# Optimization experiments

Measured on AMD Instinct MI355X. Metric: run time of the kernel, lower is better.

## Reference

```python
import jax, jax.numpy as jnp
import numpy as np

N, E = 50000, 1600000
IN_C, HEADS, OUT_C = 128, 4, 32


def setup_inputs() -> dict:
    key = jax.random.key(0)
    ks = jax.random.split(key, 8)
    x = jax.random.normal(ks[0], (N, IN_C), dtype=jnp.float32)
    row = jnp.sort(jax.random.randint(ks[1], (E,), 0, N, dtype=jnp.int32)).astype(jnp.int64)
    col = jax.random.randint(ks[2], (E,), 0, N, dtype=jnp.int64)
    # xavier_uniform-style params
    def xavier(k, shape, fan_in, fan_out):
        lim = float(np.sqrt(6.0 / (fan_in + fan_out)))
        return jax.random.uniform(k, shape, jnp.float32, -lim, lim)
    weight = xavier(ks[3], (IN_C, HEADS * OUT_C), IN_C, HEADS * OUT_C)
    att_src = xavier(ks[4], (1, HEADS, OUT_C), HEADS, OUT_C)
    att_dst = xavier(ks[5], (1, HEADS, OUT_C), HEADS, OUT_C)
    bias = jnp.zeros((HEADS * OUT_C,), jnp.float32)
    return {"x": x, "weight": weight, "att_src": att_src, "att_dst": att_dst,
            "bias": bias, "row": row, "col": col}


def reference(x, weight, att_src, att_dst, bias, row, col):
    n = x.shape[0]
    H, C = att_src.shape[1], att_src.shape[2]
    xp = (x @ weight).reshape(n, H, C)                 # [N,H,C]
    a_src = jnp.sum(xp * att_src, axis=-1)             # [N,H]
    a_dst = jnp.sum(xp * att_dst, axis=-1)             # [N,H]
    alpha = jax.nn.leaky_relu(a_src[row] + a_dst[col], negative_slope=0.2)  # [E,H]
    # torch scatter_reduce amax with include_self=True over a zeros buffer -> max(0, seg_max)
    amax = jnp.maximum(jax.ops.segment_max(alpha, row, num_segments=n), 0.0)
    alpha = jnp.exp(alpha - amax[row])
    asum = jax.ops.segment_sum(alpha, row, num_segments=n)
    alpha = alpha / (asum[row] + 1e-8)                 # [E,H]
    msg = alpha[:, :, None] * xp[col]                  # [E,H,C]
    out = jax.ops.segment_sum(msg, row, num_segments=n).reshape(n, H * C)
    return out + bias
```

## Files before the change

### kernel.cpp

```cpp
#include <hip/hip_runtime.h>
#include <hip/hip_bf16.h>


#define IN_C 128
#define HC 128
#define STG 256

typedef __attribute__((ext_vector_type(8))) __bf16 bfrag_t;
typedef __attribute__((ext_vector_type(4))) float f32x4;
union frag_u { uint4 u; bfrag_t b; };

static __device__ inline unsigned short f2bf(float f) {
    unsigned u = __float_as_uint(f);
    unsigned r = (u + 0x7fffu + ((u >> 16) & 1u)) >> 16;
    return (unsigned short)r;
}
static __device__ inline unsigned pack2(float a, float b) {
    return (unsigned)f2bf(a) | ((unsigned)f2bf(b) << 16);
}
static __device__ inline float bf_lo(unsigned u) { return __uint_as_float(u << 16); }
static __device__ inline float bf_hi(unsigned u) { return __uint_as_float(u & 0xffff0000u); }
static __device__ inline float bfu(unsigned short s) {
    return __uint_as_float((unsigned)s << 16);
}

__global__ __launch_bounds__(256) void prep_kernel(const float* __restrict__ W,
                                                   unsigned short* __restrict__ wt,
                                                   const int* __restrict__ row,
                                                   int* __restrict__ row_ptr,
                                                   int n_nodes, int E) {
    int gid = blockIdx.x * 256 + threadIdx.x;
    if (gid < IN_C * HC) {
        int n = gid >> 7, k = gid & 127;
        wt[((size_t)n * 16 + ((k >> 3) ^ (n & 7))) * 8 + (k & 7)] =
            f2bf(W[(size_t)k * HC + n]);
    }
    if (gid < E) {
        int lane = threadIdx.x & 63;
        int r1 = row[gid];
        int r0 = __shfl_up(r1, 1, 64);
        if (lane == 0) r0 = (gid == 0) ? -1 : row[gid - 1];
        for (int v = r0 + 1; v <= r1; ++v) row_ptr[v] = gid;
        if (gid == E - 1)
            for (int v = r1 + 1; v <= n_nodes; ++v) row_ptr[v] = E;
    }
}

__global__ __launch_bounds__(512) void gemm_kernel(const float* __restrict__ x,
                                                   const uint4* __restrict__ wt,
                                                   const float* __restrict__ attS,
                                                   const float* __restrict__ attD,
                                                   unsigned short* __restrict__ xp,
                                                   float* __restrict__ a_src,
                                                   float* __restrict__ a_dst, int n_nodes) {
    __shared__ uint4 Bl[2048];
    __shared__ uint4 Al[2048];
    const int tid = threadIdx.x;
    const int base = blockIdx.x * 128;

    #pragma unroll
    for (int i = 0; i < 4; ++i) Bl[tid + 512 * i] = wt[tid + 512 * i];

    #pragma unroll
    for (int i = 0; i < 4; ++i) {
        int idx = tid + 512 * i;
        int row = idx >> 4, chunk = idx & 15;
        uint4 p = make_uint4(0u, 0u, 0u, 0u);
        if (base + row < n_nodes) {
            const float* src = x + (size_t)(base + row) * IN_C + chunk * 8;
            float4 lo = *(const float4*)src;
            float4 hi = *(const float4*)(src + 4);
            p.x = pack2(lo.x, lo.y); p.y = pack2(lo.z, lo.w);
            p.z = pack2(hi.x, hi.y); p.w = pack2(hi.z, hi.w);
        }
        Al[row * 16 + (chunk ^ (row & 7))] = p;
    }
    __syncthreads();

    const int w = tid >> 6, l = tid & 63, l15 = l & 15, q = l >> 4;
    f32x4 acc[8] = {};
    const int arow = 16 * w + l15;
    #pragma unroll
    for (int ks = 0; ks < 4; ++ks) {
        frag_u a; a.u = Al[arow * 16 + ((ks * 4 + q) ^ (arow & 7))];
        #pragma unroll
        for (int t = 0; t < 8; ++t) {
            int brow = 16 * t + l15;
            frag_u b; b.u = Bl[brow * 16 + ((ks * 4 + q) ^ (brow & 7))];
            acc[t] = __builtin_amdgcn_mfma_f32_16x16x32_bf16(a.b, b.b, acc[t], 0, 0, 0);
        }
    }

    float avS[8], avD[8];
    #pragma unroll
    for (int t = 0; t < 8; ++t) {
        avS[t] = attS[16 * t + l15];
        avD[t] = attD[16 * t + l15];
    }
    float hpS[4][4] = {}, hpD[4][4] = {};
    #pragma unroll
    for (int t = 0; t < 8; ++t) {
        #pragma unroll
        for (int r = 0; r < 4; ++r) {
            float v = acc[t][r];
            hpS[r][t >> 1] = fmaf(v, avS[t], hpS[r][t >> 1]);
            hpD[r][t >> 1] = fmaf(v, avD[t], hpD[r][t >> 1]);
            int grow = base + 16 * w + 4 * q + r;
            if (grow < n_nodes)
                xp[(size_t)grow * HC + 16 * t + l15] = f2bf(v);
        }
    }
    #pragma unroll
    for (int r = 0; r < 4; ++r) {
        #pragma unroll
        for (int h = 0; h < 4; ++h) {
            #pragma unroll
            for (int off = 1; off < 16; off <<= 1) {
                hpS[r][h] += __shfl_xor(hpS[r][h], off, 64);
                hpD[r][h] += __shfl_xor(hpD[r][h], off, 64);
            }
        }
        int grow = base + 16 * w + 4 * q + r;
        if (l15 == 0 && grow < n_nodes) {
            *(float4*)(a_src + (size_t)grow * 4) =
                make_float4(hpS[r][0], hpS[r][1], hpS[r][2], hpS[r][3]);
            *(float4*)(a_dst + (size_t)grow * 4) =
                make_float4(hpD[r][0], hpD[r][1], hpD[r][2], hpD[r][3]);
        }
    }
}

__global__ __launch_bounds__(256, 8) void agg_kernel(const unsigned* __restrict__ xp,
                                                     const float* __restrict__ a_src,
                                                     const float* __restrict__ a_dst,
                                                     const int* __restrict__ col,
                                                     const int* __restrict__ row_ptr,
                                                     const float* __restrict__ bias,
                                                     float* __restrict__ out, int n_nodes) {
    __shared__ unsigned short lds_w[4][STG * 4];
    __shared__ int lds_c[4][STG];
    const int wid = threadIdx.x >> 6, lane = threadIdx.x & 63;
    const int n = blockIdx.x * 4 + wid;
    const bool alive = n < n_nodes;

    int start = 0, deg = 0;
    if (alive) { start = row_ptr[n]; deg = row_ptr[n + 1] - start; }
    const bool staged = deg <= STG;
    float4 as4 = alive ? *(const float4*)(a_src + (size_t)n * 4)
                       : make_float4(0.f, 0.f, 0.f, 0.f);

    float s0 = 0.f, s1 = 0.f, s2 = 0.f, s3 = 0.f;
    for (int i = lane; i < deg; i += 64) {
        int cc = col[start + i];
        float4 ad = *(const float4*)(a_dst + (size_t)cc * 4);
        float v0 = as4.x + ad.x, v1 = as4.y + ad.y, v2 = as4.z + ad.z, v3 = as4.w + ad.w;
        v0 = v0 > 0.f ? v0 : 0.2f * v0;  v1 = v1 > 0.f ? v1 : 0.2f * v1;
        v2 = v2 > 0.f ? v2 : 0.2f * v2;  v3 = v3 > 0.f ? v3 : 0.2f * v3;
        float w0 = __expf(v0), w1 = __expf(v1), w2 = __expf(v2), w3 = __expf(v3);
        if (staged) {
            lds_c[wid][i] = cc;
            *(uint2*)&lds_w[wid][i * 4] = make_uint2(pack2(w0, w1), pack2(w2, w3));
        }
        s0 += w0; s1 += w1; s2 += w2; s3 += w3;
    }
    #pragma unroll
    for (int off = 1; off < 64; off <<= 1) {
        s0 += __shfl_xor(s0, off, 64);
        s1 += __shfl_xor(s1, off, 64);
        s2 += __shfl_xor(s2, off, 64);
        s3 += __shfl_xor(s3, off, 64);
    }

    const int h = lane >> 4;
    const float sh = h == 0 ? s0 : h == 1 ? s1 : h == 2 ? s2 : s3;
    const float inv = 1.0f / (sh + 1e-8f);
    const unsigned* xpl = xp + lane;
    float ac0 = 0.f, ac1 = 0.f;

    if (staged) {
        const unsigned short* wr = &lds_w[wid][0];
        const int* cr = &lds_c[wid][0];
        int i = 0;
        for (; i + 8 <= deg; i += 8) {
            int c0 = cr[i+0], c1 = cr[i+1], c2 = cr[i+2], c3 = cr[i+3];
            int c4 = cr[i+4], c5 = cr[i+5], c6 = cr[i+6], c7 = cr[i+7];
            float w0 = bfu(wr[(i+0)*4+h]), w1 = bfu(wr[(i+1)*4+h]);
            float w2 = bfu(wr[(i+2)*4+h]), w3 = bfu(wr[(i+3)*4+h]);
            float w4 = bfu(wr[(i+4)*4+h]), w5 = bfu(wr[(i+5)*4+h]);
            float w6 = bfu(wr[(i+6)*4+h]), w7 = bfu(wr[(i+7)*4+h]);
            unsigned u0 = xpl[(size_t)c0 * 64];
            unsigned u1 = xpl[(size_t)c1 * 64];
            unsigned u2 = xpl[(size_t)c2 * 64];
            unsigned u3 = xpl[(size_t)c3 * 64];
            unsigned u4 = xpl[(size_t)c4 * 64];
            unsigned u5 = xpl[(size_t)c5 * 64];
            unsigned u6 = xpl[(size_t)c6 * 64];
            unsigned u7 = xpl[(size_t)c7 * 64];
            ac0 = fmaf(w0, bf_lo(u0), ac0);  ac1 = fmaf(w0, bf_hi(u0), ac1);
            ac0 = fmaf(w1, bf_lo(u1), ac0);  ac1 = fmaf(w1, bf_hi(u1), ac1);
            ac0 = fmaf(w2, bf_lo(u2), ac0);  ac1 = fmaf(w2, bf_hi(u2), ac1);
            ac0 = fmaf(w3, bf_lo(u3), ac0);  ac1 = fmaf(w3, bf_hi(u3), ac1);
            ac0 = fmaf(w4, bf_lo(u4), ac0);  ac1 = fmaf(w4, bf_hi(u4), ac1);
            ac0 = fmaf(w5, bf_lo(u5), ac0);  ac1 = fmaf(w5, bf_hi(u5), ac1);
            ac0 = fmaf(w6, bf_lo(u6), ac0);  ac1 = fmaf(w6, bf_hi(u6), ac1);
            ac0 = fmaf(w7, bf_lo(u7), ac0);  ac1 = fmaf(w7, bf_hi(u7), ac1);
        }
        for (; i < deg; ++i) {
            int c0 = cr[i];
            float w0 = bfu(wr[i*4+h]);
            unsigned u0 = xpl[(size_t)c0 * 64];
            ac0 = fmaf(w0, bf_lo(u0), ac0);  ac1 = fmaf(w0, bf_hi(u0), ac1);
        }
    } else {
        const float ash = h == 0 ? as4.x : h == 1 ? as4.y : h == 2 ? as4.z : as4.w;
        for (int i = 0; i < deg; ++i) {
            int c0 = col[start + i];
            float v = ash + a_dst[(size_t)c0 * 4 + h];
            v = v > 0.f ? v : 0.2f * v;
            float w0 = __expf(v);
            unsigned u0 = xpl[(size_t)c0 * 64];
            ac0 = fmaf(w0, bf_lo(u0), ac0);  ac1 = fmaf(w0, bf_hi(u0), ac1);
        }
    }

    if (alive) {
        float2 bv = *(const float2*)(bias + 2 * lane);
        *(float2*)(out + (size_t)n * HC + 2 * lane) =
            make_float2(ac0 * inv + bv.x, ac1 * inv + bv.y);
    }
}

extern "C" void kernel_launch(void* const* d_in, const int* in_sizes, int n_in,
                              void* d_out, int out_size, void* d_ws, size_t ws_size,
                              hipStream_t stream) {
    const float* x       = (const float*)d_in[0];
    const float* weight  = (const float*)d_in[1];
    const float* att_src = (const float*)d_in[2];
    const float* att_dst = (const float*)d_in[3];
    const float* bias    = (const float*)d_in[4];
    const int*   row     = (const int*)d_in[5];
    const int*   col     = (const int*)d_in[6];
    float* out = (float*)d_out;

    const int n_nodes = in_sizes[0] / IN_C;
    const int E = in_sizes[5];

    char* ws = (char*)d_ws;
    unsigned short* xp = (unsigned short*)ws;  ws += (size_t)n_nodes * HC * sizeof(unsigned short);
    float* a_src   = (float*)ws;               ws += (size_t)n_nodes * 4 * sizeof(float);
    float* a_dst   = (float*)ws;               ws += (size_t)n_nodes * 4 * sizeof(float);
    unsigned short* wt = (unsigned short*)ws;  ws += (size_t)IN_C * HC * sizeof(unsigned short);
    int*   row_ptr = (int*)ws;                 ws += (size_t)(n_nodes + 1) * sizeof(int);

    prep_kernel<<<(E + 255) / 256, 256, 0, stream>>>(weight, wt, row, row_ptr, n_nodes, E);
    gemm_kernel<<<(n_nodes + 127) / 128, 512, 0, stream>>>(x, (const uint4*)wt,
                                                           att_src, att_dst,
                                                           xp, a_src, a_dst, n_nodes);
    agg_kernel<<<(n_nodes + 3) / 4, 256, 0, stream>>>((const unsigned*)xp, a_src, a_dst,
                                                      col, row_ptr, bias, out, n_nodes);
}
```

Measured before the change: 82.57 us.

## Fold attention vectors into weight matrix as extra GEMM columns

Precomputes W·att_src and W·att_dst per head in the prep kernel and appends them as 16 extra bf16 columns of the transposed weight. The GEMM then yields a_src/a_dst from a ninth MFMA tile, which removes the per-element FMAs and the shuffle reductions in the epilogue. The cost is one extra MFMA tile per k-step, more LDS, and bf16 rounding of the folded weights, which changes the precision of the attention logits.

```diff
diff --git a/kernel.cpp b/kernel.cpp
--- a/kernel.cpp
+++ b/kernel.cpp
@@ -5,6 +5,7 @@
 #define IN_C 128
 #define HC 128
 #define STG 256
+#define BCOLS 144
 
 typedef __attribute__((ext_vector_type(8))) __bf16 bfrag_t;
 typedef __attribute__((ext_vector_type(4))) float f32x4;
@@ -25,6 +26,8 @@
 }
 
 __global__ __launch_bounds__(256) void prep_kernel(const float* __restrict__ W,
+                                                   const float* __restrict__ attS,
+                                                   const float* __restrict__ attD,
                                                    unsigned short* __restrict__ wt,
                                                    const int* __restrict__ row,
                                                    int* __restrict__ row_ptr,
@@ -34,6 +37,19 @@
         int n = gid >> 7, k = gid & 127;
         wt[((size_t)n * 16 + ((k >> 3) ^ (n & 7))) * 8 + (k & 7)] =
             f2bf(W[(size_t)k * HC + n]);
+    } else if (gid < IN_C * HC + 16 * IN_C) {
+        int id2 = gid - IN_C * HC;
+        int n2 = id2 >> 7, k = id2 & 127;
+        float v = 0.f;
+        if (n2 < 8) {
+            int h = n2 & 3;
+            const float* wrow = W + (size_t)k * HC + h * 32;
+            const float* av = (n2 < 4 ? attS : attD) + h * 32;
+            #pragma unroll
+            for (int c = 0; c < 32; ++c) v = fmaf(wrow[c], av[c], v);
+        }
+        int n = 128 + n2;
+        wt[((size_t)n * 16 + ((k >> 3) ^ (n & 7))) * 8 + (k & 7)] = f2bf(v);
     }
     if (gid < E) {
         int lane = threadIdx.x & 63;
@@ -48,18 +64,19 @@
 
 __global__ __launch_bounds__(512) void gemm_kernel(const float* __restrict__ x,
                                                    const uint4* __restrict__ wt,
-                                                   const float* __restrict__ attS,
-                                                   const float* __restrict__ attD,
                                                    unsigned short* __restrict__ xp,
                                                    float* __restrict__ a_src,
                                                    float* __restrict__ a_dst, int n_nodes) {
-    __shared__ uint4 Bl[2048];
+    __shared__ uint4 Bl[BCOLS * 16];
     __shared__ uint4 Al[2048];
     const int tid = threadIdx.x;
     const int base = blockIdx.x * 128;
 
     #pragma unroll
-    for (int i = 0; i < 4; ++i) Bl[tid + 512 * i] = wt[tid + 512 * i];
+    for (int i = 0; i < 5; ++i) {
+        int idx = tid + 512 * i;
+        if (idx < BCOLS * 16) Bl[idx] = wt[idx];
+    }
 
     #pragma unroll
     for (int i = 0; i < 4; ++i) {
@@ -78,54 +95,35 @@
     __syncthreads();
 
     const int w = tid >> 6, l = tid & 63, l15 = l & 15, q = l >> 4;
-    f32x4 acc[8] = {};
+    f32x4 acc[9] = {};
     const int arow = 16 * w + l15;
     #pragma unroll
     for (int ks = 0; ks < 4; ++ks) {
         frag_u a; a.u = Al[arow * 16 + ((ks * 4 + q) ^ (arow & 7))];
         #pragma unroll
-        for (int t = 0; t < 8; ++t) {
+        for (int t = 0; t < 9; ++t) {
             int brow = 16 * t + l15;
             frag_u b; b.u = Bl[brow * 16 + ((ks * 4 + q) ^ (brow & 7))];
             acc[t] = __builtin_amdgcn_mfma_f32_16x16x32_bf16(a.b, b.b, acc[t], 0, 0, 0);
         }
     }
 
-    float avS[8], avD[8];
-    #pragma unroll
-    for (int t = 0; t < 8; ++t) {
-        avS[t] = attS[16 * t + l15];
-        avD[t] = attD[16 * t + l15];
-    }
-    float hpS[4][4] = {}, hpD[4][4] = {};
     #pragma unroll
     for (int t = 0; t < 8; ++t) {
         #pragma unroll
         for (int r = 0; r < 4; ++r) {
-            float v = acc[t][r];
-            hpS[r][t >> 1] = fmaf(v, avS[t], hpS[r][t >> 1]);
-            hpD[r][t >> 1] = fmaf(v, avD[t], hpD[r][t >> 1]);
             int grow = base + 16 * w + 4 * q + r;
             if (grow < n_nodes)
-                xp[(size_t)grow * HC + 16 * t + l15] = f2bf(v);
-        }
-    }
-    #pragma unroll
-    for (int r = 0; r < 4; ++r) {
+                xp[(size_t)grow * HC + 16 * t + l15] = f2bf(acc[t][r]);
+        }
+    }
+    if (l15 < 8) {
+        float* dst = (l15 < 4) ? a_src : a_dst;
+        int hh = l15 & 3;
         #pragma unroll
-        for (int h = 0; h < 4; ++h) {
-            #pragma unroll
-            for (int off = 1; off < 16; off <<= 1) {
-                hpS[r][h] += __shfl_xor(hpS[r][h], off, 64);
-                hpD[r][h] += __shfl_xor(hpD[r][h], off, 64);
-            }
-        }
-        int grow = base + 16 * w + 4 * q + r;
-        if (l15 == 0 && grow < n_nodes) {
-            *(float4*)(a_src + (size_t)grow * 4) =
-                make_float4(hpS[r][0], hpS[r][1], hpS[r][2], hpS[r][3]);
-            *(float4*)(a_dst + (size_t)grow * 4) =
-                make_float4(hpD[r][0], hpD[r][1], hpD[r][2], hpD[r][3]);
+        for (int r = 0; r < 4; ++r) {
+            int grow = base + 16 * w + 4 * q + r;
+            if (grow < n_nodes) dst[(size_t)grow * 4 + hh] = acc[8][r];
         }
     }
 }
@@ -249,12 +247,12 @@
     unsigned short* xp = (unsigned short*)ws;  ws += (size_t)n_nodes * HC * sizeof(unsigned short);
     float* a_src   = (float*)ws;               ws += (size_t)n_nodes * 4 * sizeof(float);
     float* a_dst   = (float*)ws;               ws += (size_t)n_nodes * 4 * sizeof(float);
-    unsigned short* wt = (unsigned short*)ws;  ws += (size_t)IN_C * HC * sizeof(unsigned short);
+    unsigned short* wt = (unsigned short*)ws;  ws += (size_t)BCOLS * IN_C * sizeof(unsigned short);
     int*   row_ptr = (int*)ws;                 ws += (size_t)(n_nodes + 1) * sizeof(int);
 
-    prep_kernel<<<(E + 255) / 256, 256, 0, stream>>>(weight, wt, row, row_ptr, n_nodes, E);
+    prep_kernel<<<(E + 255) / 256, 256, 0, stream>>>(weight, att_src, att_dst, wt,
+                                                     row, row_ptr, n_nodes, E);
     gemm_kernel<<<(n_nodes + 127) / 128, 512, 0, stream>>>(x, (const uint4*)wt,
-                                                           att_src, att_dst,
                                                            xp, a_src, a_dst, n_nodes);
     agg_kernel<<<(n_nodes + 3) / 4, 256, 0, stream>>>((const unsigned*)xp, a_src, a_dst,
                                                       col, row_ptr, bias, out, n_nodes);
```

After: 79.53 us, median of 2. -3.7%, faster.
